# Kernel tuning notes

Hardware: AMD Instinct MI355X
Metric: run time of the kernel (lower is better)

The kernel has to match this reference:

```python
import jax, jax.numpy as jnp
import numpy as np
from jax import lax


def conv2d(x, w, b=None, pad=0, groups=1):
    y = lax.conv_general_dilated(x, w, (1, 1), [(pad, pad), (pad, pad)],
                                 dimension_numbers=('NCHW', 'OIHW', 'NCHW'),
                                 feature_group_count=groups)
    if b is not None:
        y = y + b[None, :, None, None]
    return y


def prelu(x, a):
    return jnp.where(x > 0, x, a * x)


def box_blur(x, k, p):
    # depthwise uniform box filter, groups=3, 'same' output size
    w = jnp.full((3, 1, k, k), 1.0 / (k * k), x.dtype)
    return conv2d(x, w, pad=p, groups=3)


def head(body, hw, hb, c1, c2):
    h = conv2d(body, hw, hb, pad=1)                      # [B,4,H,W]
    g = jnp.mean(h, axis=(2, 3), keepdims=True)          # CALayer: GAP
    s = jax.nn.sigmoid(conv2d(jax.nn.relu(conv2d(g, c1, pad=0)), c2, pad=0))
    return jax.nn.softmax(h * s, axis=1)                 # Softmax2d over channels


def fuse(x, h):
    # kernel_1 is a 1x1 identity conv -> just x
    m2 = box_blur(x, 5, 2)
    m3 = box_blur(x, 15, 7)
    m4 = box_blur(x, 25, 12)
    return h[:, 0:1] * x + h[:, 1:2] * m2 + h[:, 2:3] * m3 + h[:, 3:4] * m4


def setup_inputs() -> dict:
    key = jax.random.key(0)
    ks = jax.random.split(key, 20)
    f32 = jnp.float32
    d = {}
    d['x'] = jax.random.normal(ks[0], (8, 3, 512, 512), f32)
    # body convs
    d['bw1'] = jax.random.normal(ks[1], (32, 3, 3, 3), f32) * 0.05
    d['bb1'] = jnp.zeros((32,), f32)
    d['a1'] = jnp.full((1,), 0.25, f32)
    d['bw2'] = jax.random.normal(ks[2], (64, 32, 3, 3), f32) * 0.05
    d['bb2'] = jnp.zeros((64,), f32)
    d['a2'] = jnp.full((1,), 0.25, f32)
    d['bw3'] = jax.random.normal(ks[3], (32, 64, 3, 3), f32) * 0.05
    d['bb3'] = jnp.zeros((32,), f32)
    d['a3'] = jnp.full((1,), 0.25, f32)
    for i, k0 in zip((1, 2, 3), (4, 8, 12)):
        d[f'h{i}w'] = jax.random.normal(ks[k0], (4, 32, 3, 3), f32) * 0.05
        d[f'h{i}b'] = jnp.zeros((4,), f32)
        d[f'h{i}c1'] = jax.random.normal(ks[k0 + 1], (4, 4, 1, 1), f32) * 0.1
        d[f'h{i}c2'] = jax.random.normal(ks[k0 + 2], (4, 4, 1, 1), f32) * 0.1
    return d


def reference(x, bw1, bb1, a1, bw2, bb2, a2, bw3, bb3, a3,
              h1w, h1b, h1c1, h1c2,
              h2w, h2b, h2c1, h2c2,
              h3w, h3b, h3c1, h3c2):
    body = prelu(conv2d(x, bw1, bb1, pad=1), a1)
    body = prelu(conv2d(body, bw2, bb2, pad=1), a2)
    body = prelu(conv2d(body, bw3, bb3, pad=1), a3)
    h1 = head(body, h1w, h1b, h1c1, h1c2)
    h2 = head(body, h2w, h2b, h2c1, h2c2)
    h3 = head(body, h3w, h3b, h3c1, h3c2)
    out1 = fuse(x, h1)
    out2 = fuse(out1, h2)
    out3 = fuse(out2, h3)
    return out3
```

## Files before the change

### kernel.cpp

```cpp
#include <hip/hip_runtime.h>
#include <math.h>

#define HWSZ (512*512)

typedef unsigned int u32;
typedef __attribute__((ext_vector_type(8))) short short8;
typedef __attribute__((ext_vector_type(4))) float f32x4;

__device__ __forceinline__ unsigned short f2bf(float f) {
    unsigned u = __float_as_uint(f);
    unsigned r = (u + 0x7FFFu + ((u >> 16) & 1u)) >> 16;
    return (unsigned short)r;
}
__device__ __forceinline__ float bf2f(unsigned short h) {
    return __uint_as_float((unsigned)h << 16);
}

#define PITCH 516
#define PROWS 514
#define LDSPLANE 15360

__device__ __forceinline__ void dma16(const unsigned short* g, unsigned short* l)
{
    __builtin_amdgcn_global_load_lds(
        (const __attribute__((address_space(1))) unsigned int*)g,
        (__attribute__((address_space(3))) unsigned int*)l,
        16, 0, 0);
}

__global__ void prep_weights(const float* __restrict__ w2, const float* __restrict__ w3,
                             const float* __restrict__ hw1, const float* __restrict__ hw2,
                             const float* __restrict__ hw3,
                             const float* __restrict__ hb1, const float* __restrict__ hb2,
                             const float* __restrict__ hb3,
                             unsigned short* __restrict__ w2h, unsigned short* __restrict__ w2l,
                             unsigned short* __restrict__ w3h, unsigned short* __restrict__ w3l,
                             unsigned short* __restrict__ whh, unsigned short* __restrict__ whl,
                             float* __restrict__ hb16)
{
    int i = blockIdx.x * 256 + threadIdx.x;
    if (i < 18432) {
        int tap = i / 2048, r = i % 2048, co = r / 32, ci = r % 32;
        float v = w2[((co * 32 + ci) * 9) + tap];
        unsigned short h = f2bf(v);
        w2h[i] = h; w2l[i] = f2bf(v - bf2f(h));
    } else if (i < 36864) {
        int e = i - 18432;
        int tap = e / 2048, r = e % 2048, co = r / 64, ci = r % 64;
        float v = w3[((co * 64 + ci) * 9) + tap];
        unsigned short h = f2bf(v);
        w3h[e] = h; w3l[e] = f2bf(v - bf2f(h));
    } else if (i < 41472) {
        int e = i - 36864;
        int tap = e / 512, r = e % 512, co16 = r / 32, ci = r % 32;
        float v = 0.f;
        if (co16 < 12) {
            int hd = co16 >> 2, cl = co16 & 3;
            const float* wp = hd == 0 ? hw1 : (hd == 1 ? hw2 : hw3);
            v = wp[((cl * 32 + ci) * 9) + tap];
        }
        unsigned short h = f2bf(v);
        whh[e] = h; whl[e] = f2bf(v - bf2f(h));
    } else if (i < 41488) {
        int j = i - 41472;
        float v = 0.f;
        if (j < 12) {
            const float* bp = (j >> 2) == 0 ? hb1 : ((j >> 2) == 1 ? hb2 : hb3);
            v = bp[j & 3];
        }
        hb16[j] = v;
    }
}

__global__ void zero_border(unsigned short* __restrict__ ph,
                            unsigned short* __restrict__ pl, int logc)
{
    int i = blockIdx.x * 256 + threadIdx.x;
    const int C = 1 << logc;
    if (i >= 3080 * C) return;
    int pix = i >> logc, ch = i & (C - 1);
    int row, col;
    if (pix < 2 * PITCH) {
        row = (pix < PITCH) ? 0 : (PROWS - 1);
        col = (pix < PITCH) ? pix : pix - PITCH;
    } else {
        int q = pix - 2 * PITCH;
        row = 1 + (q >> 2);
        int c = q & 3;
        col = (c == 0) ? 0 : 512 + c;
    }
    size_t o = ((size_t)(row * PITCH + col)) * C + ch;
    ph[o] = 0;
    pl[o] = 0;
}

template<int CIN, int RB>
__device__ __forceinline__ void stage_half(const unsigned short* bp, unsigned short* ldsb)
{
    #pragma unroll
    for (int k = 0; k < 15; ++k) {
        const int rid = RB + k;
        const int r = rid / 5, cb = rid % 5;
        dma16(bp + (size_t)(r * PITCH + cb * 16) * CIN, ldsb + rid * 512);
    }
}

template<int CIN>
__device__ __forceinline__ void stage_dma(const unsigned short* __restrict__ inh,
                                          const unsigned short* __restrict__ inl,
                                          unsigned short* s_a,
                                          int w, int lane, int x1, int y0, int c0)
{
    const int c16 = lane & 15;
    const int g   = lane >> 4;
    const unsigned short* base = (w < 2) ? inh : inl;
    unsigned short* ldsb = s_a + ((w < 2) ? 0 : LDSPLANE);
    const unsigned short* bp = base
        + ((size_t)(y0 * PITCH + x1 + c16)) * CIN + c0 + g * 8;
    if (w & 1) stage_half<CIN, 15>(bp, ldsb);
    else       stage_half<CIN, 0>(bp, ldsb);
}

__device__ __forceinline__ int frag_off(int rr, int col, int quad)
{
    return ((rr * 5 + (col >> 4)) << 9) + (((quad << 4) | (col & 15)) << 3);
}

template<int CIN, int COUT>
__global__ __launch_bounds__(256, 2)
void conv_mfma(const unsigned short* __restrict__ inh, const unsigned short* __restrict__ inl,
               const unsigned short* __restrict__ wh, const unsigned short* __restrict__ wl,
               const float* __restrict__ bias, const float* __restrict__ alpha,
               unsigned short* __restrict__ outh, unsigned short* __restrict__ outl)
{
    constexpr int NTW = COUT / 16;
    __shared__ __align__(16) unsigned short s_a[2 * LDSPLANE];

    const int tid  = threadIdx.x;
    const int w    = tid >> 6;
    const int lane = tid & 63;
    const int ln   = lane & 15;
    const int quad = lane >> 4;
    const int x1   = blockIdx.x * 64;
    const int y0   = blockIdx.y * 4;

    f32x4 acc[4][NTW];
    #pragma unroll
    for (int mt = 0; mt < 4; ++mt)
        #pragma unroll
        for (int nt = 0; nt < NTW; ++nt)
            acc[mt][nt] = (f32x4){0.f, 0.f, 0.f, 0.f};

    for (int c0 = 0; c0 < CIN; c0 += 32) {
        if (c0) __syncthreads();
        stage_dma<CIN>(inh, inl, s_a, w, lane, x1, y0, c0);
        asm volatile("s_waitcnt vmcnt(0)" ::: "memory");
        __syncthreads();

        #pragma unroll
        for (int tap = 0; tap < 9; ++tap) {
            const int dy = tap / 3, dx = tap % 3;
            short8 bh[NTW], bl[NTW];
            #pragma unroll
            for (int nt = 0; nt < NTW; ++nt) {
                size_t off = ((size_t)(tap * COUT + nt * 16 + ln)) * CIN + c0 + quad * 8;
                bh[nt] = *(const short8*)(wh + off);
                bl[nt] = *(const short8*)(wl + off);
            }
            short8 ah[4], al[4];
            #pragma unroll
            for (int mt = 0; mt < 4; ++mt) {
                const int mti = w * 4 + mt;
                const int rr  = (mti >> 2) + dy;
                const int col = ((mti & 3) << 4) + ln + dx;
                const int off = frag_off(rr, col, quad);
                ah[mt] = *(const short8*)(s_a + off);
                al[mt] = *(const short8*)(s_a + LDSPLANE + off);
            }
            #pragma unroll
            for (int mt = 0; mt < 4; ++mt)
                #pragma unroll
                for (int nt = 0; nt < NTW; ++nt)
                    acc[mt][nt] = __builtin_amdgcn_mfma_f32_16x16x32_bf16(ah[mt], bh[nt], acc[mt][nt], 0, 0, 0);
            #pragma unroll
            for (int mt = 0; mt < 4; ++mt)
                #pragma unroll
                for (int nt = 0; nt < NTW; ++nt)
                    acc[mt][nt] = __builtin_amdgcn_mfma_f32_16x16x32_bf16(al[mt], bh[nt], acc[mt][nt], 0, 0, 0);
            #pragma unroll
            for (int mt = 0; mt < 4; ++mt)
                #pragma unroll
                for (int nt = 0; nt < NTW; ++nt)
                    acc[mt][nt] = __builtin_amdgcn_mfma_f32_16x16x32_bf16(ah[mt], bl[nt], acc[mt][nt], 0, 0, 0);
        }
    }

    const float av = alpha[0];
    float bs[NTW];
    #pragma unroll
    for (int nt = 0; nt < NTW; ++nt) bs[nt] = bias[nt * 16 + ln];
    #pragma unroll
    for (int mt = 0; mt < 4; ++mt) {
        const int mti = w * 4 + mt;
        const int y   = y0 + (mti >> 2);
        const int xb  = x1 + ((mti & 3) << 4) + quad * 4;
        #pragma unroll
        for (int nt = 0; nt < NTW; ++nt) {
            const int co = nt * 16 + ln;
            #pragma unroll
            for (int reg = 0; reg < 4; ++reg) {
                float t = acc[mt][nt][reg] + bs[nt];
                t = t > 0.f ? t : av * t;
                unsigned short hh = f2bf(t);
                unsigned short ll = f2bf(t - bf2f(hh));
                size_t o = ((size_t)((y + 1) * PITCH + xb + reg + 1)) * COUT + co;
                outh[o] = hh;
                outl[o] = ll;
            }
        }
    }
}

__global__ __launch_bounds__(256, 2)
void head_mfma(const unsigned short* __restrict__ inh, const unsigned short* __restrict__ inl,
               const unsigned short* __restrict__ wh, const unsigned short* __restrict__ wl,
               const float* __restrict__ hb,
               float* __restrict__ h, float* __restrict__ g2, int b)
{
    __shared__ __align__(16) unsigned short s_a[2 * LDSPLANE];
    __shared__ float s_red[4][16];

    const int tid  = threadIdx.x;
    const int w    = tid >> 6;
    const int lane = tid & 63;
    const int ln   = lane & 15;
    const int quad = lane >> 4;
    const int x1   = blockIdx.x * 64;
    const int y0   = blockIdx.y * 4;

    f32x4 acc[4];
    #pragma unroll
    for (int mt = 0; mt < 4; ++mt) acc[mt] = (f32x4){0.f, 0.f, 0.f, 0.f};

    stage_dma<32>(inh, inl, s_a, w, lane, x1, y0, 0);
    asm volatile("s_waitcnt vmcnt(0)" ::: "memory");
    __syncthreads();

    #pragma unroll
    for (int tap = 0; tap < 9; ++tap) {
        const int dy = tap / 3, dx = tap % 3;
        size_t boff = (size_t)tap * 512 + ln * 32 + quad * 8;
        short8 bh = *(const short8*)(wh + boff);
        short8 bl = *(const short8*)(wl + boff);
        short8 ah[4], al[4];
        #pragma unroll
        for (int mt = 0; mt < 4; ++mt) {
            const int mti = w * 4 + mt;
            const int rr  = (mti >> 2) + dy;
            const int col = ((mti & 3) << 4) + ln + dx;
            const int off = frag_off(rr, col, quad);
            ah[mt] = *(const short8*)(s_a + off);
            al[mt] = *(const short8*)(s_a + LDSPLANE + off);
        }
        #pragma unroll
        for (int mt = 0; mt < 4; ++mt)
            acc[mt] = __builtin_amdgcn_mfma_f32_16x16x32_bf16(ah[mt], bh, acc[mt], 0, 0, 0);
        #pragma unroll
        for (int mt = 0; mt < 4; ++mt)
            acc[mt] = __builtin_amdgcn_mfma_f32_16x16x32_bf16(al[mt], bh, acc[mt], 0, 0, 0);
        #pragma unroll
        for (int mt = 0; mt < 4; ++mt)
            acc[mt] = __builtin_amdgcn_mfma_f32_16x16x32_bf16(ah[mt], bl, acc[mt], 0, 0, 0);
    }

    __syncthreads();
    float* s_h = (float*)s_a;
    const float bs = hb[ln];
    float psum = 0.f;
    #pragma unroll
    for (int mt = 0; mt < 4; ++mt) {
        const int mti  = w * 4 + mt;
        const int base = (mti >> 2) * 64 + ((mti & 3) << 4) + quad * 4;
        #pragma unroll
        for (int reg = 0; reg < 4; ++reg) {
            float v = acc[mt][reg] + bs;
            if (ln < 12) s_h[ln * 260 + base + reg] = v;
            psum += v;
        }
    }
    psum += __shfl_down(psum, 16);
    psum += __shfl_down(psum, 32);
    if (lane < 16) s_red[w][lane] = psum;
    __syncthreads();

    if (tid < 192) {
        const int co = tid >> 4, ch = tid & 15;
        const float* src = s_h + co * 260 + ch * 16;
        float4 v0 = *(const float4*)(src);
        float4 v1 = *(const float4*)(src + 4);
        float4 v2 = *(const float4*)(src + 8);
        float4 v3 = *(const float4*)(src + 12);
        const int hd = co >> 2, cl = co & 3;
        float* dst = h + ((size_t)((hd * 8 + b) * 4 + cl)) * HWSZ
                       + (size_t)(y0 + (ch >> 2)) * 512 + x1 + ((ch & 3) << 4);
        *(float4*)(dst)      = v0;
        *(float4*)(dst + 4)  = v1;
        *(float4*)(dst + 8)  = v2;
        *(float4*)(dst + 12) = v3;
    }
    if (tid < 12) {
        float t = s_red[0][tid] + s_red[1][tid] + s_red[2][tid] + s_red[3][tid];
        atomicAdd(&g2[(tid >> 2) * 32 + b * 4 + (tid & 3)], t);
    }
}

__global__ __launch_bounds__(256)
void conv1_nhwc(const float* __restrict__ x, const float* __restrict__ wgt,
                const float* __restrict__ bias, const float* __restrict__ alpha,
                unsigned short* __restrict__ outh, unsigned short* __restrict__ outl)
{
    __shared__ float s_in[3][6][72];
    __shared__ float s_w[3][9][32];
    __shared__ float s_b[32];
    const int tid = threadIdx.x;
    const int x1 = blockIdx.x * 64, y0 = blockIdx.y * 4;

    for (int i = tid; i < 3 * 6 * 66; i += 256) {
        int ci = i / 396, rm = i % 396;
        int r = rm / 66, cc = rm % 66;
        int gy = y0 - 1 + r, gx = x1 - 1 + cc;
        float v = 0.f;
        if ((unsigned)gy < 512u && (unsigned)gx < 512u)
            v = x[(size_t)ci * HWSZ + gy * 512 + gx];
        s_in[ci][r][cc] = v;
    }
    for (int i = tid; i < 864; i += 256) {
        int co = i & 31, rm = i >> 5;
        int ci = rm / 9, tap = rm % 9;
        s_w[ci][tap][co] = wgt[(co * 3 + ci) * 9 + tap];
    }
    if (tid < 32) s_b[tid] = bias[tid];
    __syncthreads();

    const int ty = tid >> 6, tx = tid & 63;
    float acc[32];
    #pragma unroll
    for (int i = 0; i < 32; ++i) acc[i] = 0.f;
    #pragma unroll
    for (int ci = 0; ci < 3; ++ci)
        #pragma unroll
        for (int tap = 0; tap < 9; ++tap) {
            const int dy = tap / 3, dx = tap % 3;
            float iv = s_in[ci][ty + dy][tx + dx];
            #pragma unroll
            for (int c4 = 0; c4 < 8; ++c4) {
                float4 wv = *(const float4*)&s_w[ci][tap][c4 * 4];
                acc[c4*4+0] = fmaf(iv, wv.x, acc[c4*4+0]);
                acc[c4*4+1] = fmaf(iv, wv.y, acc[c4*4+1]);
                acc[c4*4+2] = fmaf(iv, wv.z, acc[c4*4+2]);
                acc[c4*4+3] = fmaf(iv, wv.w, acc[c4*4+3]);
            }
        }
    const float av = alpha[0];
    u32 ph[16], pl[16];
    #pragma unroll
    for (int cp = 0; cp < 16; ++cp) {
        float t0 = acc[2*cp]     + s_b[2*cp];     t0 = t0 > 0.f ? t0 : av * t0;
        float t1 = acc[2*cp + 1] + s_b[2*cp + 1]; t1 = t1 > 0.f ? t1 : av * t1;
        unsigned short h0 = f2bf(t0), h1 = f2bf(t1);
        unsigned short l0 = f2bf(t0 - bf2f(h0)), l1 = f2bf(t1 - bf2f(h1));
        ph[cp] = (u32)h0 | ((u32)h1 << 16);
        pl[cp] = (u32)l0 | ((u32)l1 << 16);
    }
    size_t o = ((size_t)((y0 + ty + 1) * PITCH + x1 + tx + 1)) * 32;
    #pragma unroll
    for (int q = 0; q < 4; ++q) {
        *(uint4*)(outh + o + q * 8) = (uint4){ph[4*q], ph[4*q+1], ph[4*q+2], ph[4*q+3]};
        *(uint4*)(outl + o + q * 8) = (uint4){pl[4*q], pl[4*q+1], pl[4*q+2], pl[4*q+3]};
    }
}

__global__ void zero_k(float* p, int n)
{
    int i = blockIdx.x * 256 + threadIdx.x;
    if (i < n) p[i] = 0.f;
}

__global__ void ca_kernel(const float* __restrict__ g,
                          const float* __restrict__ c11, const float* __restrict__ c12,
                          const float* __restrict__ c21, const float* __restrict__ c22,
                          const float* __restrict__ c31, const float* __restrict__ c32,
                          float* __restrict__ sOut)
{
    int t = threadIdx.x;
    if (t >= 24) return;
    int head = t / 8, b = t % 8;
    const float* c1 = head == 0 ? c11 : (head == 1 ? c21 : c31);
    const float* c2 = head == 0 ? c12 : (head == 1 ? c22 : c32);
    float m[4], v[4];
    #pragma unroll
    for (int i = 0; i < 4; ++i) m[i] = g[head * 32 + b * 4 + i] * (1.0f / 262144.0f);
    #pragma unroll
    for (int j = 0; j < 4; ++j) {
        float xv = c1[j*4+0]*m[0] + c1[j*4+1]*m[1] + c1[j*4+2]*m[2] + c1[j*4+3]*m[3];
        v[j] = fmaxf(xv, 0.f);
    }
    #pragma unroll
    for (int j = 0; j < 4; ++j) {
        float xv = c2[j*4+0]*v[0] + c2[j*4+1]*v[1] + c2[j*4+2]*v[2] + c2[j*4+3]*v[3];
        sOut[head * 32 + b * 4 + j] = 1.f / (1.f + __expf(-xv));
    }
}

__global__ __launch_bounds__(256)
void sat_row(const float* __restrict__ src, float* __restrict__ S)
{
    const int y  = blockIdx.x;
    const int bc = blockIdx.y;
    float* Sp = S + (size_t)bc * 263169;
    const int tid = threadIdx.x;
    if (y == 0) {
        for (int i = tid; i < 513; i += 256) Sp[i] = 0.f;
        return;
    }
    const float2* row2 = (const float2*)(src + (size_t)bc * HWSZ + (size_t)(y - 1) * 512);
    float2 ab = row2[tid];
    float ps = ab.x + ab.y;
    float v = ps;
    const int lane = tid & 63;
    #pragma unroll
    for (int off = 1; off < 64; off <<= 1) {
        float u = __shfl_up(v, off);
        if (lane >= off) v += u;
    }
    __shared__ float wsum[4];
    const int wv = tid >> 6;
    if (lane == 63) wsum[wv] = v;
    __syncthreads();
    float woff = 0.f;
    #pragma unroll
    for (int k = 0; k < 4; ++k) if (k < wv) woff += wsum[k];
    float excl = woff + v - ps;
    float* o = Sp + (size_t)y * 513;
    if (tid == 0) o[0] = 0.f;
    o[1 + 2 * tid] = excl + ab.x;
    o[2 + 2 * tid] = excl + ab.x + ab.y;
}

__global__ __launch_bounds__(256)
void sat_col(float* __restrict__ S)
{
    const int bc = blockIdx.x;
    const int c  = 1 + blockIdx.y * 256 + threadIdx.x;
    float* P = S + (size_t)bc * 263169 + c;
    float run = 0.f;
    for (int r0 = 1; r0 <= 512; r0 += 16) {
        float v[16];
        #pragma unroll
        for (int i = 0; i < 16; ++i) v[i] = P[(size_t)(r0 + i) * 513];
        #pragma unroll
        for (int i = 0; i < 16; ++i) { run += v[i]; v[i] = run; }
        #pragma unroll
        for (int i = 0; i < 16; ++i) P[(size_t)(r0 + i) * 513] = v[i];
    }
}

__device__ __forceinline__ float boxsum(const float* __restrict__ S, int y, int x, int p)
{
    int y0 = max(y - p, 0), x0 = max(x - p, 0);
    int y1 = min(y + p, 511) + 1, x1 = min(x + p, 511) + 1;
    return S[y1 * 513 + x1] - S[y0 * 513 + x1] - S[y1 * 513 + x0] + S[y0 * 513 + x0];
}

__global__ __launch_bounds__(256)
void fuse_kernel(const float* __restrict__ cur, const float* __restrict__ h,
                 const float* __restrict__ sv, const float* __restrict__ S,
                 float* __restrict__ out, int head)
{
    const int idx = blockIdx.x * 256 + threadIdx.x;
    const int b   = idx >> 18;
    const int rem = idx & 262143;
    const int y   = rem >> 9;
    const int x   = rem & 511;

    const float* sp = sv + head * 32 + b * 4;
    const float* hp = h + (size_t)((head * 8 + b) * 4) * HWSZ + rem;
    float z0 = hp[0]          * sp[0];
    float z1 = hp[HWSZ]       * sp[1];
    float z2 = hp[2 * HWSZ]   * sp[2];
    float z3 = hp[3 * HWSZ]   * sp[3];
    float m  = fmaxf(fmaxf(z0, z1), fmaxf(z2, z3));
    float e0 = __expf(z0 - m), e1 = __expf(z1 - m), e2 = __expf(z2 - m), e3 = __expf(z3 - m);
    float inv = 1.f / (e0 + e1 + e2 + e3);
    float p0 = e0 * inv, p1 = e1 * inv, p2 = e2 * inv, p3 = e3 * inv;

    #pragma unroll
    for (int c = 0; c < 3; ++c) {
        const float* Sp = S + (size_t)(b * 3 + c) * 263169;
        float xv = cur[((size_t)b * 3 + c) * HWSZ + rem];
        float m2 = boxsum(Sp, y, x, 2)  * (1.f / 25.f);
        float m3 = boxsum(Sp, y, x, 7)  * (1.f / 225.f);
        float m4 = boxsum(Sp, y, x, 12) * (1.f / 625.f);
        out[((size_t)b * 3 + c) * HWSZ + rem] = p0 * xv + p1 * m2 + p2 * m3 + p3 * m4;
    }
}

extern "C" void kernel_launch(void* const* d_in, const int* in_sizes, int n_in,
                              void* d_out, int out_size, void* d_ws, size_t ws_size,
                              hipStream_t stream)
{
    (void)in_sizes; (void)n_in; (void)out_size; (void)ws_size;
    const float* x    = (const float*)d_in[0];
    const float* bw1  = (const float*)d_in[1];
    const float* bb1  = (const float*)d_in[2];
    const float* a1   = (const float*)d_in[3];
    const float* bw2  = (const float*)d_in[4];
    const float* bb2  = (const float*)d_in[5];
    const float* a2   = (const float*)d_in[6];
    const float* bw3  = (const float*)d_in[7];
    const float* bb3  = (const float*)d_in[8];
    const float* a3   = (const float*)d_in[9];
    const float* h1w  = (const float*)d_in[10];
    const float* h1b  = (const float*)d_in[11];
    const float* h1c1 = (const float*)d_in[12];
    const float* h1c2 = (const float*)d_in[13];
    const float* h2w  = (const float*)d_in[14];
    const float* h2b  = (const float*)d_in[15];
    const float* h2c1 = (const float*)d_in[16];
    const float* h2c2 = (const float*)d_in[17];
    const float* h3w  = (const float*)d_in[18];
    const float* h3b  = (const float*)d_in[19];
    const float* h3c1 = (const float*)d_in[20];
    const float* h3c2 = (const float*)d_in[21];

    const size_t T1P = (size_t)PROWS * PITCH * 32;
    const size_t T2P = (size_t)PROWS * PITCH * 64;

    unsigned short* t1h = (unsigned short*)d_ws;
    unsigned short* t1l = t1h + T1P;
    unsigned short* t2h = t1l + T1P;
    unsigned short* t2l = t2h + T2P;
    float* hbuf = (float*)(t2l + T2P);
    float* gbuf = hbuf + 25165824;
    float* sbuf = gbuf + 96;
    unsigned short* wb = (unsigned short*)(sbuf + 96);
    unsigned short* w2h = wb;
    unsigned short* w2l = wb + 18432;
    unsigned short* w3h = wb + 36864;
    unsigned short* w3l = wb + 55296;
    unsigned short* whh = wb + 73728;
    unsigned short* whl = wb + 78336;
    float* hb16 = (float*)(wb + 82944);
    float* SAT  = (float*)t2h;
    float* ping = (float*)t1h;

    dim3 blk(256);

    prep_weights<<<dim3(163), blk, 0, stream>>>(bw2, bw3, h1w, h2w, h3w,
                                                h1b, h2b, h3b,
                                                w2h, w2l, w3h, w3l, whh, whl, hb16);
    zero_k<<<dim3(1), dim3(128), 0, stream>>>(gbuf, 96);
    zero_border<<<dim3(385), blk, 0, stream>>>(t1h, t1l, 5);
    zero_border<<<dim3(770), blk, 0, stream>>>(t2h, t2l, 6);

    for (int b = 0; b < 8; ++b) {
        conv1_nhwc<<<dim3(8, 128), blk, 0, stream>>>(x + (size_t)b * 3 * HWSZ,
                                                     bw1, bb1, a1, t1h, t1l);
        conv_mfma<32, 64><<<dim3(8, 128), blk, 0, stream>>>(t1h, t1l, w2h, w2l, bb2, a2, t2h, t2l);
        conv_mfma<64, 32><<<dim3(8, 128), blk, 0, stream>>>(t2h, t2l, w3h, w3l, bb3, a3, t1h, t1l);
        head_mfma<<<dim3(8, 128), blk, 0, stream>>>(t1h, t1l, whh, whl, hb16, hbuf, gbuf, b);
    }

    ca_kernel<<<dim3(1), dim3(64), 0, stream>>>(gbuf, h1c1, h1c2, h2c1, h2c2,
                                                h3c1, h3c2, sbuf);

    const float* cur = x;
    for (int i = 0; i < 3; ++i) {
        sat_row<<<dim3(513, 24), blk, 0, stream>>>(cur, SAT);
        sat_col<<<dim3(24, 2), blk, 0, stream>>>(SAT);
        float* nxt = (i == 2) ? (float*)d_out : ping;
        fuse_kernel<<<dim3(8192), blk, 0, stream>>>(cur, hbuf, sbuf, SAT, nxt, i);
        cur = nxt;
    }
}
```

Measured before the change: 1.515 ms.

## Restructure body convs: stage hi/lo planes sequentially, full-CIN tiles, LDS-staged coalesced stores

Replaces the generic conv_mfma with conv_body. It stages the whole input-channel depth of one precision plane at a time: the hi plane first, computing hi*whi and hi*wlo, then the lo plane computing lo*whi. This shrinks the LDS footprint for the 32->64 conv, so that kernel can raise its launch bound to 4 blocks per SM, and it reuses each A fragment across both weight planes. The epilogue now writes hi/lo outputs through LDS and stores them as 16-byte coalesced vectors instead of scattered 2-byte stores. The cost is extra barriers and a second, serialized staging phase per block.

Measured after the change: 1.746 ms. 15.2% more time.

```diff
diff --git a/kernel.cpp b/kernel.cpp
--- a/kernel.cpp
+++ b/kernel.cpp
@@ -94,6 +94,171 @@
     pl[o] = 0;
 }
 
+template<int CIN>
+__device__ __forceinline__ void stage_plane(const unsigned short* __restrict__ src,
+                                            unsigned short* s_a,
+                                            int w, int lane, int x1, int y0)
+{
+    const int c16 = lane & 15;
+    const int q   = lane >> 4;
+    if constexpr (CIN == 64) {
+        #pragma unroll
+        for (int k = 0; k < 15; ++k) {
+            const int u = w * 15 + k;
+            const int r = u / 10, rem = u % 10;
+            const int cb = rem >> 1, gh = rem & 1;
+            const unsigned short* g = src
+                + ((size_t)((y0 + r) * PITCH + x1 + cb * 16 + c16)) * 64 + gh * 32 + q * 8;
+            dma16(g, s_a + u * 512);
+        }
+    } else {
+        #pragma unroll
+        for (int k = 0; k < 8; ++k) {
+            const int u = w + 4 * k;
+            if (u < 30) {
+                const int r = u / 5, cb = u % 5;
+                const unsigned short* g = src
+                    + ((size_t)((y0 + r) * PITCH + x1 + cb * 16 + c16)) * 32 + q * 8;
+                dma16(g, s_a + u * 512);
+            }
+        }
+    }
+}
+
+template<int CIN, int COUT, bool BOTH>
+__device__ __forceinline__ void compute_chunk(const unsigned short* s_a,
+    const unsigned short* __restrict__ wh, const unsigned short* __restrict__ wl,
+    f32x4 (&acc)[4][COUT/16], int w, int ln, int quad)
+{
+    constexpr int KS  = CIN / 32;
+    constexpr int NTW = COUT / 16;
+    #pragma unroll
+    for (int tap = 0; tap < 9; ++tap) {
+        const int dy = tap / 3, dx = tap % 3;
+        #pragma unroll
+        for (int ks = 0; ks < KS; ++ks) {
+            short8 a[4];
+            #pragma unroll
+            for (int mt = 0; mt < 4; ++mt) {
+                const int mti = w * 4 + mt;
+                const int rr  = (mti >> 2) + dy;
+                const int col = ((mti & 3) << 4) + ln + dx;
+                const int off = (((rr * 5 + (col >> 4)) * KS + ks) << 9)
+                              + (((quad << 4) | (col & 15)) << 3);
+                a[mt] = *(const short8*)(s_a + off);
+            }
+            #pragma unroll
+            for (int nt = 0; nt < NTW; ++nt) {
+                const size_t woff = ((size_t)(tap * COUT + nt * 16 + ln)) * CIN
+                                  + ks * 32 + quad * 8;
+                short8 bh = *(const short8*)(wh + woff);
+                #pragma unroll
+                for (int mt = 0; mt < 4; ++mt)
+                    acc[mt][nt] = __builtin_amdgcn_mfma_f32_16x16x32_bf16(a[mt], bh, acc[mt][nt], 0, 0, 0);
+                if constexpr (BOTH) {
+                    short8 bl = *(const short8*)(wl + woff);
+                    #pragma unroll
+                    for (int mt = 0; mt < 4; ++mt)
+                        acc[mt][nt] = __builtin_amdgcn_mfma_f32_16x16x32_bf16(a[mt], bl, acc[mt][nt], 0, 0, 0);
+                }
+            }
+        }
+    }
+}
+
+template<int CIN, int COUT>
+__device__ __forceinline__ void conv_body(
+    const unsigned short* __restrict__ inh, const unsigned short* __restrict__ inl,
+    const unsigned short* __restrict__ wh, const unsigned short* __restrict__ wl,
+    const float* __restrict__ bias, const float* __restrict__ alpha,
+    unsigned short* __restrict__ outh, unsigned short* __restrict__ outl,
+    unsigned short* s_a)
+{
+    constexpr int NTW = COUT / 16;
+    const int tid  = threadIdx.x;
+    const int w    = tid >> 6;
+    const int lane = tid & 63;
+    const int ln   = lane & 15;
+    const int quad = lane >> 4;
+    const int x1   = blockIdx.x * 64;
+    const int y0   = blockIdx.y * 4;
+
+    f32x4 acc[4][NTW];
+    #pragma unroll
+    for (int mt = 0; mt < 4; ++mt)
+        #pragma unroll
+        for (int nt = 0; nt < NTW; ++nt)
+            acc[mt][nt] = (f32x4){0.f, 0.f, 0.f, 0.f};
+
+    stage_plane<CIN>(inh, s_a, w, lane, x1, y0);
+    asm volatile("s_waitcnt vmcnt(0)" ::: "memory");
+    __syncthreads();
+    compute_chunk<CIN, COUT, true>(s_a, wh, wl, acc, w, ln, quad);
+    __syncthreads();
+
+    stage_plane<CIN>(inl, s_a, w, lane, x1, y0);
+    asm volatile("s_waitcnt vmcnt(0)" ::: "memory");
+    __syncthreads();
+    compute_chunk<CIN, COUT, false>(s_a, wh, wl, acc, w, ln, quad);
+
+    const float av = alpha[0];
+    float bs[NTW];
+    #pragma unroll
+    for (int nt = 0; nt < NTW; ++nt) bs[nt] = bias[nt * 16 + ln];
+
+    #pragma unroll
+    for (int plane = 0; plane < 2; ++plane) {
+        __syncthreads();
+        #pragma unroll
+        for (int mt = 0; mt < 4; ++mt) {
+            const int mti = w * 4 + mt;
+            const int r   = mti >> 2;
+            const int cb  = (mti & 3) << 4;
+            #pragma unroll
+            for (int nt = 0; nt < NTW; ++nt) {
+                #pragma unroll
+                for (int reg = 0; reg < 4; ++reg) {
+                    float t = acc[mt][nt][reg] + bs[nt];
+                    t = t > 0.f ? t : av * t;
+                    unsigned short hh = f2bf(t);
+                    unsigned short v = plane ? f2bf(t - bf2f(hh)) : hh;
+                    s_a[(r * 64 + cb + (quad << 2) + reg) * COUT + nt * 16 + ln] = v;
+                }
+            }
+        }
+        __syncthreads();
+        unsigned short* op = plane ? outl : outh;
+        #pragma unroll
+        for (int it = 0; it < COUT / 8; ++it) {
+            const int L = (it * 256 + tid) * 8;
+            const int r = L / (64 * COUT);
+            const int inner = L - r * (64 * COUT);
+            const size_t go = ((size_t)((y0 + r + 1) * PITCH + x1 + 1)) * COUT + inner;
+            *(uint4*)(op + go) = *(const uint4*)(s_a + L);
+        }
+    }
+}
+
+__global__ __launch_bounds__(256, 4)
+void conv_mfma_c2(const unsigned short* __restrict__ inh, const unsigned short* __restrict__ inl,
+                  const unsigned short* __restrict__ wh, const unsigned short* __restrict__ wl,
+                  const float* __restrict__ bias, const float* __restrict__ alpha,
+                  unsigned short* __restrict__ outh, unsigned short* __restrict__ outl)
+{
+    __shared__ __align__(16) unsigned short s_a[16384];
+    conv_body<32, 64>(inh, inl, wh, wl, bias, alpha, outh, outl, s_a);
+}
+
+__global__ __launch_bounds__(256, 2)
+void conv_mfma_c3(const unsigned short* __restrict__ inh, const unsigned short* __restrict__ inl,
+                  const unsigned short* __restrict__ wh, const unsigned short* __restrict__ wl,
+                  const float* __restrict__ bias, const float* __restrict__ alpha,
+                  unsigned short* __restrict__ outh, unsigned short* __restrict__ outl)
+{
+    __shared__ __align__(16) unsigned short s_a[30720];
+    conv_body<64, 32>(inh, inl, wh, wl, bias, alpha, outh, outl, s_a);
+}
+
 template<int CIN, int RB>
 __device__ __forceinline__ void stage_half(const unsigned short* bp, unsigned short* ldsb)
 {
@@ -124,101 +289,6 @@
 __device__ __forceinline__ int frag_off(int rr, int col, int quad)
 {
     return ((rr * 5 + (col >> 4)) << 9) + (((quad << 4) | (col & 15)) << 3);
-}
-
-template<int CIN, int COUT>
-__global__ __launch_bounds__(256, 2)
-void conv_mfma(const unsigned short* __restrict__ inh, const unsigned short* __restrict__ inl,
-               const unsigned short* __restrict__ wh, const unsigned short* __restrict__ wl,
-               const float* __restrict__ bias, const float* __restrict__ alpha,
-               unsigned short* __restrict__ outh, unsigned short* __restrict__ outl)
-{
-    constexpr int NTW = COUT / 16;
-    __shared__ __align__(16) unsigned short s_a[2 * LDSPLANE];
-
-    const int tid  = threadIdx.x;
-    const int w    = tid >> 6;
-    const int lane = tid & 63;
-    const int ln   = lane & 15;
-    const int quad = lane >> 4;
-    const int x1   = blockIdx.x * 64;
-    const int y0   = blockIdx.y * 4;
-
-    f32x4 acc[4][NTW];
-    #pragma unroll
-    for (int mt = 0; mt < 4; ++mt)
-        #pragma unroll
-        for (int nt = 0; nt < NTW; ++nt)
-            acc[mt][nt] = (f32x4){0.f, 0.f, 0.f, 0.f};
-
-    for (int c0 = 0; c0 < CIN; c0 += 32) {
-        if (c0) __syncthreads();
-        stage_dma<CIN>(inh, inl, s_a, w, lane, x1, y0, c0);
-        asm volatile("s_waitcnt vmcnt(0)" ::: "memory");
-        __syncthreads();
-
-        #pragma unroll
-        for (int tap = 0; tap < 9; ++tap) {
-            const int dy = tap / 3, dx = tap % 3;
-            short8 bh[NTW], bl[NTW];
-            #pragma unroll
-            for (int nt = 0; nt < NTW; ++nt) {
-                size_t off = ((size_t)(tap * COUT + nt * 16 + ln)) * CIN + c0 + quad * 8;
-                bh[nt] = *(const short8*)(wh + off);
-                bl[nt] = *(const short8*)(wl + off);
-            }
-            short8 ah[4], al[4];
-            #pragma unroll
-            for (int mt = 0; mt < 4; ++mt) {
-                const int mti = w * 4 + mt;
-                const int rr  = (mti >> 2) + dy;
-                const int col = ((mti & 3) << 4) + ln + dx;
-                const int off = frag_off(rr, col, quad);
-                ah[mt] = *(const short8*)(s_a + off);
-                al[mt] = *(const short8*)(s_a + LDSPLANE + off);
-            }
-            #pragma unroll
-            for (int mt = 0; mt < 4; ++mt)
-                #pragma unroll
-                for (int nt = 0; nt < NTW; ++nt)
-                    acc[mt][nt] = __builtin_amdgcn_mfma_f32_16x16x32_bf16(ah[mt], bh[nt], acc[mt][nt], 0, 0, 0);
-            #pragma unroll
-            for (int mt = 0; mt < 4; ++mt)
-                #pragma unroll
-                for (int nt = 0; nt < NTW; ++nt)
-                    acc[mt][nt] = __builtin_amdgcn_mfma_f32_16x16x32_bf16(al[mt], bh[nt], acc[mt][nt], 0, 0, 0);
-            #pragma unroll
-            for (int mt = 0; mt < 4; ++mt)
-                #pragma unroll
-                for (int nt = 0; nt < NTW; ++nt)
-                    acc[mt][nt] = __builtin_amdgcn_mfma_f32_16x16x32_bf16(ah[mt], bl[nt], acc[mt][nt], 0, 0, 0);
-        }
-    }
-
-    const float av = alpha[0];
-    float bs[NTW];
-    #pragma unroll
-    for (int nt = 0; nt < NTW; ++nt) bs[nt] = bias[nt * 16 + ln];
-    #pragma unroll
-    for (int mt = 0; mt < 4; ++mt) {
-        const int mti = w * 4 + mt;
-        const int y   = y0 + (mti >> 2);
-        const int xb  = x1 + ((mti & 3) << 4) + quad * 4;
-        #pragma unroll
-        for (int nt = 0; nt < NTW; ++nt) {
-            const int co = nt * 16 + ln;
-            #pragma unroll
-            for (int reg = 0; reg < 4; ++reg) {
-                float t = acc[mt][nt][reg] + bs[nt];
-                t = t > 0.f ? t : av * t;
-                unsigned short hh = f2bf(t);
-                unsigned short ll = f2bf(t - bf2f(hh));
-                size_t o = ((size_t)((y + 1) * PITCH + xb + reg + 1)) * COUT + co;
-                outh[o] = hh;
-                outl[o] = ll;
-            }
-        }
-    }
 }
 
 __global__ __launch_bounds__(256, 2)
@@ -566,8 +636,8 @@
     for (int b = 0; b < 8; ++b) {
         conv1_nhwc<<<dim3(8, 128), blk, 0, stream>>>(x + (size_t)b * 3 * HWSZ,
                                                      bw1, bb1, a1, t1h, t1l);
-        conv_mfma<32, 64><<<dim3(8, 128), blk, 0, stream>>>(t1h, t1l, w2h, w2l, bb2, a2, t2h, t2l);
-        conv_mfma<64, 32><<<dim3(8, 128), blk, 0, stream>>>(t2h, t2l, w3h, w3l, bb3, a3, t1h, t1l);
+        conv_mfma_c2<<<dim3(8, 128), blk, 0, stream>>>(t1h, t1l, w2h, w2l, bb2, a2, t2h, t2l);
+        conv_mfma_c3<<<dim3(8, 128), blk, 0, stream>>>(t2h, t2l, w3h, w3l, bb3, a3, t1h, t1l);
         head_mfma<<<dim3(8, 128), blk, 0, stream>>>(t1h, t1l, whh, whl, hb16, hbuf, gbuf, b);
     }
 
```
